# Kernel optimization log

Hardware: AMD Instinct MI355X
Metric: run time of the kernel (lower is better)

## Reference

```python
import jax, jax.numpy as jnp
import numpy as np

# Block sizes (DGL message-flow-graph / sampled blocks)
NS0, ND0, NE0 = 300000, 50000, 800000   # block0: 2-hop frontier -> 1-hop frontier
NS1, ND1, NE1 = 50000, 8192, 131072     # block1: 1-hop frontier -> seed nodes


def _graph_conv(x, src, dst, ew, W, b, n_src, n_dst, weight_first):
    """DGL GraphConv with norm='both' and edge_weight.

    x: [n_src, d_in] source-node features; (src, dst): edge endpoints;
    ew: [E] edge weights. Degrees are UNWEIGHTED (copy of DGL semantics),
    clamped to >= 1. Weight applied before aggregation iff d_in > d_out.
    """
    ones_e = jnp.ones_like(ew)
    out_deg = jnp.clip(jax.ops.segment_sum(ones_e, src, num_segments=n_src), 1.0, None)
    h = x * (out_deg ** -0.5)[:, None]
    if weight_first:
        h = h @ W
    # gather-weight-scatter: m_v = sum_{e: e->v} ew_e * h_{src_e}
    msg = jax.ops.segment_sum(ew[:, None] * h[src], dst, num_segments=n_dst)
    in_deg = jnp.clip(jax.ops.segment_sum(ones_e, dst, num_segments=n_dst), 1.0, None)
    msg = msg * (in_deg ** -0.5)[:, None]
    if not weight_first:
        msg = msg @ W
    return msg + b


def setup_inputs() -> dict:
    key = jax.random.key(0)
    ks = jax.random.split(key, 12)
    in_f, hid_f, out_f = 256, 128, 128
    return {
        "x": jax.random.normal(ks[0], (NS0, in_f), dtype=jnp.float32),
        "src0": jax.random.randint(ks[1], (NE0,), 0, NS0, dtype=jnp.int64 if jax.config.jax_enable_x64 else jnp.int32).astype(jnp.int32),
        "dst0": jax.random.randint(ks[2], (NE0,), 0, ND0).astype(jnp.int32),
        "ew0": jax.random.normal(ks[3], (NE0,), dtype=jnp.float32),
        "src1": jax.random.randint(ks[4], (NE1,), 0, NS1).astype(jnp.int32),
        "dst1": jax.random.randint(ks[5], (NE1,), 0, ND1).astype(jnp.int32),
        "ew1": jax.random.normal(ks[6], (NE1,), dtype=jnp.float32),
        "W1": jax.random.normal(ks[7], (in_f, hid_f), dtype=jnp.float32) * 0.05,
        "b1": jax.random.normal(ks[8], (hid_f,), dtype=jnp.float32) * 0.05,
        "W2": jax.random.normal(ks[9], (hid_f, out_f), dtype=jnp.float32) * 0.05,
        "b2": jax.random.normal(ks[10], (out_f,), dtype=jnp.float32) * 0.05,
    }


def reference(x, src0, dst0, ew0, src1, dst1, ew1, W1, b1, W2, b2):
    # layer 1: in(256) > hidden(128) -> weight applied before aggregation
    h = jax.nn.relu(_graph_conv(x, src0, dst0, ew0, W1, b1, NS0, ND0, weight_first=True))
    # layer 2: hidden(128) <= out(128) -> aggregate then weight
    out = jax.nn.relu(_graph_conv(h, src1, dst1, ew1, W2, b2, NS1, ND1, weight_first=False))
    return out  # [ND1, out_f]
```

## Files before the change

### kernel.cpp

```cpp
#include <hip/hip_runtime.h>

#define NS0 300000
#define ND0 50000
#define NE0 800000
#define NS1 50000
#define ND1 8192
#define NE1 131072
#define IN_F 256
#define HID_F 128
#define SLOTS 64

#define OFF_OUTDEG0I 0
#define OFF_OUTDEG1I 300000
#define OFF_CNT0     350000
#define OFF_CNT1     400000
#define ZERO_WORDS   408192
#define OFF_EDGE0    408192
#define OFF_EDGE1    6808192
#define OFF_H1       7856768

__global__ __launch_bounds__(256) void k_zero(int4* __restrict__ p, int n4) {
  int i = blockIdx.x * 256 + threadIdx.x;
  int s = gridDim.x * 256;
  for (; i < n4; i += s) p[i] = make_int4(0, 0, 0, 0);
}

__global__ __launch_bounds__(256) void k_build(
    const int* __restrict__ src0, const int* __restrict__ dst0,
    const float* __restrict__ ew0, int* __restrict__ outdeg0,
    int* __restrict__ cnt0, int2* __restrict__ edge0,
    const int* __restrict__ src1, const int* __restrict__ dst1,
    const float* __restrict__ ew1, int* __restrict__ outdeg1,
    int* __restrict__ cnt1, int2* __restrict__ edge1) {
  int tid = blockIdx.x * blockDim.x + threadIdx.x;
  int stride = gridDim.x * blockDim.x;
  for (int i = tid; i < NE0; i += stride) {
    int s = src0[i];
    int d = dst0[i];
    float w = ew0[i];
    atomicAdd(&outdeg0[s], 1);
    int slot = atomicAdd(&cnt0[d], 1);
    if (slot < SLOTS) edge0[d * SLOTS + slot] = make_int2(s, __float_as_int(w));
  }
  for (int i = tid; i < NE1; i += stride) {
    int s = src1[i];
    int d = dst1[i];
    float w = ew1[i];
    atomicAdd(&outdeg1[s], 1);
    int slot = atomicAdd(&cnt1[d], 1);
    if (slot < SLOTS) edge1[d * SLOTS + slot] = make_int2(s, __float_as_int(w));
  }
}

#define FMA4(acc, c, v)        \
  acc.x = fmaf(c, v.x, acc.x); \
  acc.y = fmaf(c, v.y, acc.y); \
  acc.z = fmaf(c, v.z, acc.z); \
  acc.w = fmaf(c, v.w, acc.w);

#define COEF(sr, wbits) \
  (__int_as_float(wbits) * rsqrtf(fmaxf((float)outdeg[sr], 1.0f)))

__global__ __launch_bounds__(256) void k_layer1(
    const float* __restrict__ x, const int* __restrict__ cnt,
    const int* __restrict__ outdeg, const int2* __restrict__ edge,
    const float* __restrict__ W1, const float* __restrict__ b1,
    float* __restrict__ h1) {
  __shared__ float arow[8][IN_F];
  const int t = blockIdx.x;
  const int wv = threadIdx.x >> 6;
  const int lane = threadIdx.x & 63;

#pragma unroll
  for (int rr = 0; rr < 2; ++rr) {
    const int row = t * 8 + wv * 2 + rr;
    const int deg = min(cnt[row], SLOTS);
    const int2* ep = edge + (size_t)row * SLOTS;
    float4 acc = make_float4(0.f, 0.f, 0.f, 0.f);
    int e = 0;
    for (; e + 4 <= deg; e += 4) {
      int4 q0 = *reinterpret_cast<const int4*>(ep + e);
      int4 q1 = *reinterpret_cast<const int4*>(ep + e + 2);
      float4 v0 = *reinterpret_cast<const float4*>(x + (size_t)q0.x * IN_F + lane * 4);
      float4 v1 = *reinterpret_cast<const float4*>(x + (size_t)q0.z * IN_F + lane * 4);
      float4 v2 = *reinterpret_cast<const float4*>(x + (size_t)q1.x * IN_F + lane * 4);
      float4 v3 = *reinterpret_cast<const float4*>(x + (size_t)q1.z * IN_F + lane * 4);
      float c0 = COEF(q0.x, q0.y);
      float c1 = COEF(q0.z, q0.w);
      float c2 = COEF(q1.x, q1.y);
      float c3 = COEF(q1.z, q1.w);
      FMA4(acc, c0, v0);
      FMA4(acc, c1, v1);
      FMA4(acc, c2, v2);
      FMA4(acc, c3, v3);
    }
    for (; e < deg; ++e) {
      int2 p = ep[e];
      float4 v = *reinterpret_cast<const float4*>(x + (size_t)p.x * IN_F + lane * 4);
      float c = COEF(p.x, p.y);
      FMA4(acc, c, v);
    }
    const float sc = rsqrtf(fmaxf((float)deg, 1.0f));
    *reinterpret_cast<float4*>(&arow[wv * 2 + rr][lane * 4]) =
        make_float4(acc.x * sc, acc.y * sc, acc.z * sc, acc.w * sc);
  }
  __syncthreads();

  const int j = threadIdx.x & 127;
  const int rg = threadIdx.x >> 7;
  float a0 = 0.f, a1 = 0.f, a2 = 0.f, a3 = 0.f;
  const float* wj = W1 + j;
#pragma unroll 8
  for (int k = 0; k < IN_F; ++k) {
    const float wvv = wj[(size_t)k * 128];
    a0 = fmaf(arow[rg * 4 + 0][k], wvv, a0);
    a1 = fmaf(arow[rg * 4 + 1][k], wvv, a1);
    a2 = fmaf(arow[rg * 4 + 2][k], wvv, a2);
    a3 = fmaf(arow[rg * 4 + 3][k], wvv, a3);
  }
  const float bj = b1[j];
  const int row0 = t * 8 + rg * 4;
  h1[(size_t)(row0 + 0) * 128 + j] = fmaxf(a0 + bj, 0.0f);
  h1[(size_t)(row0 + 1) * 128 + j] = fmaxf(a1 + bj, 0.0f);
  h1[(size_t)(row0 + 2) * 128 + j] = fmaxf(a2 + bj, 0.0f);
  h1[(size_t)(row0 + 3) * 128 + j] = fmaxf(a3 + bj, 0.0f);
}

#define FMA2(acc, c, v)        \
  acc.x = fmaf(c, v.x, acc.x); \
  acc.y = fmaf(c, v.y, acc.y);

__global__ __launch_bounds__(256) void k_layer2(
    const float* __restrict__ h1, const int* __restrict__ cnt,
    const int* __restrict__ outdeg, const int2* __restrict__ edge,
    const float* __restrict__ W2, const float* __restrict__ b2,
    float* __restrict__ out) {
  __shared__ float arow[8][HID_F];
  const int t = blockIdx.x;
  const int wv = threadIdx.x >> 6;
  const int lane = threadIdx.x & 63;

#pragma unroll
  for (int rr = 0; rr < 2; ++rr) {
    const int row = t * 8 + wv * 2 + rr;
    const int deg = min(cnt[row], SLOTS);
    const int2* ep = edge + (size_t)row * SLOTS;
    float2 acc = make_float2(0.f, 0.f);
    int e = 0;
    for (; e + 4 <= deg; e += 4) {
      int4 q0 = *reinterpret_cast<const int4*>(ep + e);
      int4 q1 = *reinterpret_cast<const int4*>(ep + e + 2);
      float2 v0 = *reinterpret_cast<const float2*>(h1 + (size_t)q0.x * HID_F + lane * 2);
      float2 v1 = *reinterpret_cast<const float2*>(h1 + (size_t)q0.z * HID_F + lane * 2);
      float2 v2 = *reinterpret_cast<const float2*>(h1 + (size_t)q1.x * HID_F + lane * 2);
      float2 v3 = *reinterpret_cast<const float2*>(h1 + (size_t)q1.z * HID_F + lane * 2);
      float c0 = COEF(q0.x, q0.y);
      float c1 = COEF(q0.z, q0.w);
      float c2 = COEF(q1.x, q1.y);
      float c3 = COEF(q1.z, q1.w);
      FMA2(acc, c0, v0);
      FMA2(acc, c1, v1);
      FMA2(acc, c2, v2);
      FMA2(acc, c3, v3);
    }
    for (; e < deg; ++e) {
      int2 p = ep[e];
      float2 v = *reinterpret_cast<const float2*>(h1 + (size_t)p.x * HID_F + lane * 2);
      float c = COEF(p.x, p.y);
      FMA2(acc, c, v);
    }
    const float sc = rsqrtf(fmaxf((float)deg, 1.0f));
    *reinterpret_cast<float2*>(&arow[wv * 2 + rr][lane * 2]) =
        make_float2(acc.x * sc, acc.y * sc);
  }
  __syncthreads();

  const int j = threadIdx.x & 127;
  const int rg = threadIdx.x >> 7;
  float a0 = 0.f, a1 = 0.f, a2 = 0.f, a3 = 0.f;
  const float* wj = W2 + j;
#pragma unroll 8
  for (int k = 0; k < HID_F; ++k) {
    const float wvv = wj[(size_t)k * 128];
    a0 = fmaf(arow[rg * 4 + 0][k], wvv, a0);
    a1 = fmaf(arow[rg * 4 + 1][k], wvv, a1);
    a2 = fmaf(arow[rg * 4 + 2][k], wvv, a2);
    a3 = fmaf(arow[rg * 4 + 3][k], wvv, a3);
  }
  const float bj = b2[j];
  const int row0 = t * 8 + rg * 4;
  out[(size_t)(row0 + 0) * 128 + j] = fmaxf(a0 + bj, 0.0f);
  out[(size_t)(row0 + 1) * 128 + j] = fmaxf(a1 + bj, 0.0f);
  out[(size_t)(row0 + 2) * 128 + j] = fmaxf(a2 + bj, 0.0f);
  out[(size_t)(row0 + 3) * 128 + j] = fmaxf(a3 + bj, 0.0f);
}

extern "C" void kernel_launch(void* const* d_in, const int* in_sizes, int n_in,
                              void* d_out, int out_size, void* d_ws, size_t ws_size,
                              hipStream_t stream) {
  const float* x    = (const float*)d_in[0];
  const int*   src0 = (const int*)d_in[1];
  const int*   dst0 = (const int*)d_in[2];
  const float* ew0  = (const float*)d_in[3];
  const int*   src1 = (const int*)d_in[4];
  const int*   dst1 = (const int*)d_in[5];
  const float* ew1  = (const float*)d_in[6];
  const float* W1   = (const float*)d_in[7];
  const float* b1   = (const float*)d_in[8];
  const float* W2   = (const float*)d_in[9];
  const float* b2   = (const float*)d_in[10];
  float* out = (float*)d_out;

  int*   wsi = (int*)d_ws;
  float* wsf = (float*)d_ws;
  int* outdeg0 = wsi + OFF_OUTDEG0I;
  int* outdeg1 = wsi + OFF_OUTDEG1I;
  int* cnt0    = wsi + OFF_CNT0;
  int* cnt1    = wsi + OFF_CNT1;
  int2* edge0  = (int2*)(wsi + OFF_EDGE0);
  int2* edge1  = (int2*)(wsi + OFF_EDGE1);
  float* h1    = wsf + OFF_H1;

  k_zero<<<128, 256, 0, stream>>>((int4*)d_ws, ZERO_WORDS / 4);
  k_build<<<1024, 256, 0, stream>>>(src0, dst0, ew0, outdeg0, cnt0, edge0,
                                    src1, dst1, ew1, outdeg1, cnt1, edge1);
  k_layer1<<<ND0 / 8, 256, 0, stream>>>(x, cnt0, outdeg0, edge0, W1, b1, h1);
  k_layer2<<<ND1 / 8, 256, 0, stream>>>(h1, cnt1, outdeg1, edge1, W2, b2, out);
}
```

Baseline: 276.5 us.

## Pre-scale and convert source features to fp16, fold degree norms into producers

Adds a pass that multiplies every source row of x by its inverse-sqrt out-degree and stores it as fp16, so the layer-1 gather reads half the bytes and skips the per-edge degree lookup. The layer-1 epilogue also pre-multiplies h1 by the layer-2 source out-degree norm, so layer 2 no longer looks up degrees per edge either. The trade-off is a full extra read of x plus an fp16 write before the gather, and fp16 rounding error on the input features.

```diff
diff --git a/kernel.cpp b/kernel.cpp
--- a/kernel.cpp
+++ b/kernel.cpp
@@ -10,6 +10,8 @@
 #define HID_F 128
 #define SLOTS 64
 
+typedef __attribute__((ext_vector_type(4))) _Float16 half4_t;
+
 #define OFF_OUTDEG0I 0
 #define OFF_OUTDEG1I 300000
 #define OFF_CNT0     350000
@@ -18,6 +20,7 @@
 #define OFF_EDGE0    408192
 #define OFF_EDGE1    6808192
 #define OFF_H1       7856768
+#define OFF_XH       14256768
 
 __global__ __launch_bounds__(256) void k_zero(int4* __restrict__ p, int n4) {
   int i = blockIdx.x * 256 + threadIdx.x;
@@ -52,18 +55,30 @@
   }
 }
 
-#define FMA4(acc, c, v)        \
-  acc.x = fmaf(c, v.x, acc.x); \
-  acc.y = fmaf(c, v.y, acc.y); \
-  acc.z = fmaf(c, v.z, acc.z); \
-  acc.w = fmaf(c, v.w, acc.w);
-
-#define COEF(sr, wbits) \
-  (__int_as_float(wbits) * rsqrtf(fmaxf((float)outdeg[sr], 1.0f)))
+__global__ __launch_bounds__(256) void k_cvt(
+    const float4* __restrict__ x4, const int* __restrict__ outdeg0,
+    half4_t* __restrict__ xh4) {
+  const int i = blockIdx.x * 256 + threadIdx.x;
+  const int row = i >> 6;
+  const float s = rsqrtf(fmaxf((float)outdeg0[row], 1.0f));
+  float4 v = x4[i];
+  half4_t o;
+  o.x = (_Float16)(v.x * s);
+  o.y = (_Float16)(v.y * s);
+  o.z = (_Float16)(v.z * s);
+  o.w = (_Float16)(v.w * s);
+  xh4[i] = o;
+}
+
+#define FMA4H(acc, c, v)                  \
+  acc.x = fmaf(c, (float)v.x, acc.x);     \
+  acc.y = fmaf(c, (float)v.y, acc.y);     \
+  acc.z = fmaf(c, (float)v.z, acc.z);     \
+  acc.w = fmaf(c, (float)v.w, acc.w);
 
 __global__ __launch_bounds__(256) void k_layer1(
-    const float* __restrict__ x, const int* __restrict__ cnt,
-    const int* __restrict__ outdeg, const int2* __restrict__ edge,
+    const _Float16* __restrict__ xh, const int* __restrict__ cnt,
+    const int2* __restrict__ edge, const int* __restrict__ outdeg1,
     const float* __restrict__ W1, const float* __restrict__ b1,
     float* __restrict__ h1) {
   __shared__ float arow[8][IN_F];
@@ -81,24 +96,19 @@
     for (; e + 4 <= deg; e += 4) {
       int4 q0 = *reinterpret_cast<const int4*>(ep + e);
       int4 q1 = *reinterpret_cast<const int4*>(ep + e + 2);
-      float4 v0 = *reinterpret_cast<const float4*>(x + (size_t)q0.x * IN_F + lane * 4);
-      float4 v1 = *reinterpret_cast<const float4*>(x + (size_t)q0.z * IN_F + lane * 4);
-      float4 v2 = *reinterpret_cast<const float4*>(x + (size_t)q1.x * IN_F + lane * 4);
-      float4 v3 = *reinterpret_cast<const float4*>(x + (size_t)q1.z * IN_F + lane * 4);
-      float c0 = COEF(q0.x, q0.y);
-      float c1 = COEF(q0.z, q0.w);
-      float c2 = COEF(q1.x, q1.y);
-      float c3 = COEF(q1.z, q1.w);
-      FMA4(acc, c0, v0);
-      FMA4(acc, c1, v1);
-      FMA4(acc, c2, v2);
-      FMA4(acc, c3, v3);
+      half4_t v0 = *reinterpret_cast<const half4_t*>(xh + (size_t)q0.x * IN_F + lane * 4);
+      half4_t v1 = *reinterpret_cast<const half4_t*>(xh + (size_t)q0.z * IN_F + lane * 4);
+      half4_t v2 = *reinterpret_cast<const half4_t*>(xh + (size_t)q1.x * IN_F + lane * 4);
+      half4_t v3 = *reinterpret_cast<const half4_t*>(xh + (size_t)q1.z * IN_F + lane * 4);
+      FMA4H(acc, __int_as_float(q0.y), v0);
+      FMA4H(acc, __int_as_float(q0.w), v1);
+      FMA4H(acc, __int_as_float(q1.y), v2);
+      FMA4H(acc, __int_as_float(q1.w), v3);
     }
     for (; e < deg; ++e) {
       int2 p = ep[e];
-      float4 v = *reinterpret_cast<const float4*>(x + (size_t)p.x * IN_F + lane * 4);
-      float c = COEF(p.x, p.y);
-      FMA4(acc, c, v);
+      half4_t v = *reinterpret_cast<const half4_t*>(xh + (size_t)p.x * IN_F + lane * 4);
+      FMA4H(acc, __int_as_float(p.y), v);
     }
     const float sc = rsqrtf(fmaxf((float)deg, 1.0f));
     *reinterpret_cast<float4*>(&arow[wv * 2 + rr][lane * 4]) =
@@ -120,10 +130,13 @@
   }
   const float bj = b1[j];
   const int row0 = t * 8 + rg * 4;
-  h1[(size_t)(row0 + 0) * 128 + j] = fmaxf(a0 + bj, 0.0f);
-  h1[(size_t)(row0 + 1) * 128 + j] = fmaxf(a1 + bj, 0.0f);
-  h1[(size_t)(row0 + 2) * 128 + j] = fmaxf(a2 + bj, 0.0f);
-  h1[(size_t)(row0 + 3) * 128 + j] = fmaxf(a3 + bj, 0.0f);
+#pragma unroll
+  for (int r = 0; r < 4; ++r) {
+    const float av = (r == 0) ? a0 : (r == 1) ? a1 : (r == 2) ? a2 : a3;
+    const int row = row0 + r;
+    const float s1 = rsqrtf(fmaxf((float)outdeg1[row], 1.0f));
+    h1[(size_t)row * 128 + j] = fmaxf(av + bj, 0.0f) * s1;
+  }
 }
 
 #define FMA2(acc, c, v)        \
@@ -132,9 +145,8 @@
 
 __global__ __launch_bounds__(256) void k_layer2(
     const float* __restrict__ h1, const int* __restrict__ cnt,
-    const int* __restrict__ outdeg, const int2* __restrict__ edge,
-    const float* __restrict__ W2, const float* __restrict__ b2,
-    float* __restrict__ out) {
+    const int2* __restrict__ edge, const float* __restrict__ W2,
+    const float* __restrict__ b2, float* __restrict__ out) {
   __shared__ float arow[8][HID_F];
   const int t = blockIdx.x;
   const int wv = threadIdx.x >> 6;
@@ -154,20 +166,15 @@
       float2 v1 = *reinterpret_cast<const float2*>(h1 + (size_t)q0.z * HID_F + lane * 2);
       float2 v2 = *reinterpret_cast<const float2*>(h1 + (size_t)q1.x * HID_F + lane * 2);
       float2 v3 = *reinterpret_cast<const float2*>(h1 + (size_t)q1.z * HID_F + lane * 2);
-      float c0 = COEF(q0.x, q0.y);
-      float c1 = COEF(q0.z, q0.w);
-      float c2 = COEF(q1.x, q1.y);
-      float c3 = COEF(q1.z, q1.w);
-      FMA2(acc, c0, v0);
-      FMA2(acc, c1, v1);
-      FMA2(acc, c2, v2);
-      FMA2(acc, c3, v3);
+      FMA2(acc, __int_as_float(q0.y), v0);
+      FMA2(acc, __int_as_float(q0.w), v1);
+      FMA2(acc, __int_as_float(q1.y), v2);
+      FMA2(acc, __int_as_float(q1.w), v3);
     }
     for (; e < deg; ++e) {
       int2 p = ep[e];
       float2 v = *reinterpret_cast<const float2*>(h1 + (size_t)p.x * HID_F + lane * 2);
-      float c = COEF(p.x, p.y);
-      FMA2(acc, c, v);
+      FMA2(acc, __int_as_float(p.y), v);
     }
     const float sc = rsqrtf(fmaxf((float)deg, 1.0f));
     *reinterpret_cast<float2*>(&arow[wv * 2 + rr][lane * 2]) =
@@ -220,10 +227,13 @@
   int2* edge0  = (int2*)(wsi + OFF_EDGE0);
   int2* edge1  = (int2*)(wsi + OFF_EDGE1);
   float* h1    = wsf + OFF_H1;
+  _Float16* xh = (_Float16*)(wsi + OFF_XH);
 
   k_zero<<<128, 256, 0, stream>>>((int4*)d_ws, ZERO_WORDS / 4);
   k_build<<<1024, 256, 0, stream>>>(src0, dst0, ew0, outdeg0, cnt0, edge0,
                                     src1, dst1, ew1, outdeg1, cnt1, edge1);
-  k_layer1<<<ND0 / 8, 256, 0, stream>>>(x, cnt0, outdeg0, edge0, W1, b1, h1);
-  k_layer2<<<ND1 / 8, 256, 0, stream>>>(h1, cnt1, outdeg1, edge1, W2, b2, out);
-}
+  k_cvt<<<NS0 * IN_F / 4 / 256, 256, 0, stream>>>(
+      (const float4*)x, outdeg0, (half4_t*)xh);
+  k_layer1<<<ND0 / 8, 256, 0, stream>>>(xh, cnt0, edge0, outdeg1, W1, b1, h1);
+  k_layer2<<<ND1 / 8, 256, 0, stream>>>(h1, cnt1, edge1, W2, b2, out);
+}
```

Result: slower. 318.3 us (+15.1%).
